# Kernel tuning notes

Hardware: AMD Instinct MI355X
Metric: run time of the kernel (lower is better)

The kernel has to match this reference:

```python
import jax, jax.numpy as jnp
import numpy as np

TOPN = 1000
MIN_SCORE = 0.05
NMS_THR = 0.5
MAX_OBJ = 100
B, A, C = 8, 100000, 80


def setup_inputs():
    key = jax.random.key(0)
    k1, k2, k3, k4 = jax.random.split(key, 4)
    cls_heads = jax.random.uniform(k1, (B, A, C), dtype=jnp.float32)  # sigmoid-like class scores
    reg_heads = (jax.random.normal(k2, (B, A, 4), dtype=jnp.float32) * 0.1)  # small tx,ty,tw,th
    ctr = jax.random.uniform(k3, (B, A, 2), minval=32.0, maxval=768.0)
    wh = jax.random.uniform(k4, (B, A, 2), minval=16.0, maxval=128.0)
    batch_anchors = jnp.concatenate([ctr - 0.5 * wh, ctr + 0.5 * wh], axis=-1)
    return {"cls_heads": cls_heads, "reg_heads": reg_heads, "batch_anchors": batch_anchors}


def _decode(reg, anchors):
    # snap tx,ty,tw,th to x1y1x2y2; original casts to int (truncation toward zero)
    awh = anchors[..., 2:4] - anchors[..., 0:2]
    actr = anchors[..., 0:2] + 0.5 * awh
    pwh = jnp.exp(reg[..., 2:4]) * awh
    pctr = reg[..., 0:2] * awh + actr
    boxes = jnp.concatenate([pctr - 0.5 * pwh, pctr + 0.5 * pwh], axis=-1)
    return jnp.trunc(boxes)  # matches torch .int() truncation, kept float


def _per_image(scores, classes, boxes):
    # score-threshold filter + descending sort + topn, done as masked top_k (fixed shapes)
    masked = jnp.where(scores > MIN_SCORE, scores, -jnp.inf)
    top_s, idx = jax.lax.top_k(masked, TOPN)
    valid = top_s > MIN_SCORE
    top_c = classes[idx].astype(jnp.float32)
    top_b = boxes[idx]  # [TOPN,4]

    # pairwise IoU (greedy python_nms math)
    wh = top_b[:, 2:4] - top_b[:, 0:2]
    area = jnp.clip(wh[:, 0] * wh[:, 1], 1e-4)  # clamp(min=0.0001)
    tl = jnp.maximum(top_b[:, None, 0:2], top_b[None, :, 0:2])
    br = jnp.minimum(top_b[:, None, 2:4], top_b[None, :, 2:4])
    sz = jnp.clip(br - tl, 0.0)
    inter = sz[..., 0] * sz[..., 1]
    union = jnp.clip(area[:, None] + area[None, :] - inter, 1e-4)
    iou = inter / union  # [TOPN,TOPN]

    ar = jnp.arange(TOPN)

    def body(i, supp):
        # box i, if not already suppressed, suppresses later boxes with iou >= thr
        return supp | ((~supp[i]) & (iou[i] >= NMS_THR) & (ar > i))

    supp = jax.lax.fori_loop(0, TOPN, body, ~valid)
    kept = (~supp) & valid

    # compact first MAX_OBJ kept detections (score order preserved); pad with -1 / zeros
    rank = jnp.cumsum(kept) - 1
    slot = jnp.where(kept & (rank < MAX_OBJ), rank, MAX_OBJ)  # dump slot MAX_OBJ
    out_s = jnp.full((MAX_OBJ + 1,), -1.0, jnp.float32).at[slot].set(jnp.where(kept, top_s, -1.0))[:MAX_OBJ]
    out_c = jnp.full((MAX_OBJ + 1,), -1.0, jnp.float32).at[slot].set(jnp.where(kept, top_c, -1.0))[:MAX_OBJ]
    out_b = jnp.zeros((MAX_OBJ + 1, 4), jnp.float32).at[slot].set(jnp.where(kept[:, None], top_b, 0.0))[:MAX_OBJ]
    return out_s, out_c, out_b


def reference(cls_heads, reg_heads, batch_anchors):
    scores = jnp.max(cls_heads, axis=2)        # [B,A]
    classes = jnp.argmax(cls_heads, axis=2)    # [B,A] int
    boxes = _decode(reg_heads, batch_anchors)  # [B,A,4]
    return jax.vmap(_per_image)(scores, classes, boxes)
```

## Files before the change

### kernel.cpp

```cpp
#include <hip/hip_runtime.h>
#include <cstdint>

#define NB 8
#define NA 100000
#define NC 80
#define TOPN 1000
#define MAXOBJ 100
#define CAND_CAP 2048
#define MIN_SCORE 0.05f
#define NMS_THR 0.5f

__global__ __launch_bounds__(320) void k_scores(const float* __restrict__ cls,
                                                unsigned int* __restrict__ keys,
                                                int* __restrict__ clsid) {
    __shared__ float sval[320];
    __shared__ int sidx[320];
    const int b = blockIdx.y;
    const int a0 = blockIdx.x * 16;
    const int t = threadIdx.x;
    const float4* base = (const float4*)(cls + ((size_t)b * NA + a0) * NC);
    float4 v = base[t];
    float m = v.x; int ix = 0;
    if (v.y > m) { m = v.y; ix = 1; }
    if (v.z > m) { m = v.z; ix = 2; }
    if (v.w > m) { m = v.w; ix = 3; }
    const int e = t % 20;
    sval[t] = m;
    sidx[t] = e * 4 + ix;
    __syncthreads();
    if (t < 16) {
        float vm = sval[t * 20]; int vi = sidx[t * 20];
        for (int i = 1; i < 20; ++i) {
            float x = sval[t * 20 + i];
            if (x > vm) { vm = x; vi = sidx[t * 20 + i]; }
        }
        size_t o = (size_t)b * NA + a0 + t;
        keys[o] = (vm > MIN_SCORE) ? __float_as_uint(vm) : 0u;
        clsid[o] = vi;
    }
}

__device__ inline void wave_agg_hist(unsigned int* lh, int bin, bool pred) {
    unsigned long long active = __ballot(pred);
    const int lane = threadIdx.x & 63;
    while (active) {
        int leader = (int)__builtin_ctzll(active);
        int lbin = __shfl(bin, leader);
        unsigned long long mask = __ballot(pred && (bin == lbin));
        if (lane == leader) atomicAdd(&lh[lbin], (unsigned int)__popcll(mask));
        active &= ~mask;
    }
}

__device__ inline void top_threshold(const unsigned int* lh, int nbins, int minbin,
                                     unsigned int rank, int* out_bin, unsigned int* out_above) {
    const int lane = threadIdx.x;
    const int chunk = nbins >> 6;
    const int hi = nbins - 1 - lane * chunk;
    const int lo = hi - chunk + 1;
    unsigned int s = 0;
    for (int i = hi; i >= lo; --i)
        if (i >= minbin) s += lh[i];
    unsigned int incl = s;
    for (int d = 1; d < 64; d <<= 1) {
        unsigned int o = __shfl_up(incl, d);
        if (lane >= d) incl += o;
    }
    unsigned int pre = incl - s;
    bool hit = (pre < rank) && (incl >= rank);
    unsigned long long m = __ballot(hit);
    if (m == 0ull) {
        if (lane == 0) { *out_bin = -1; *out_above = 0; }
        return;
    }
    if (hit) {
        unsigned int cum = pre;
        int fb = -1;
        for (int i = hi; i >= lo; --i) {
            if (i < minbin) break;
            unsigned int c = lh[i];
            if (cum + c >= rank) { fb = i; break; }
            cum += c;
        }
        *out_bin = fb;
        *out_above = cum;
    }
}

__global__ __launch_bounds__(1024) void k_mega(
    const unsigned int* __restrict__ keys, const int* __restrict__ clsid,
    const float* __restrict__ reg, const float* __restrict__ anch,
    float* __restrict__ out) {
    __shared__ unsigned int lh[2048];
    __shared__ unsigned long long sk[CAND_CAP];
    __shared__ float4 sbox[TOPN];
    __shared__ float ss[TOPN];
    __shared__ float scl[TOPN];
    __shared__ int s_bin;
    __shared__ unsigned int s_above;
    __shared__ unsigned int s_cnt;

    const int b = blockIdx.x;
    const int tid = threadIdx.x;
    const int lane = tid & 63;
    const unsigned int* kb = keys + (size_t)b * NA;
    float* out_s = out + b * MAXOBJ;
    float* out_c = out + NB * MAXOBJ + b * MAXOBJ;
    float* out_b = out + 2 * NB * MAXOBJ + b * MAXOBJ * 4;

    if (tid < MAXOBJ) { out_s[tid] = -1.0f; out_c[tid] = -1.0f; }
    if (tid < MAXOBJ * 4) out_b[tid] = 0.0f;

    for (int i = tid; i < 2048; i += 1024) lh[i] = 0;
    __syncthreads();
    for (int base = 0; base < NA; base += 1024) {
        int a = base + tid;
        bool p = a < NA;
        unsigned int key = p ? kb[a] : 0u;
        wave_agg_hist(lh, (int)(key >> 21), p);
    }
    __syncthreads();
    if (tid < 64) top_threshold(lh, 2048, 1, TOPN, &s_bin, &s_above);
    __syncthreads();
    const int p1 = s_bin;
    const unsigned int above1 = s_above;

    unsigned int T;
    if (p1 < 0) {
        T = 1u;
    } else {
        __syncthreads();
        for (int i = tid; i < 2048; i += 1024) lh[i] = 0;
        __syncthreads();
        for (int base = 0; base < NA; base += 1024) {
            int a = base + tid;
            if (a < NA) {
                unsigned int key = kb[a];
                if ((int)(key >> 21) == p1) atomicAdd(&lh[(key >> 10) & 0x7FFu], 1u);
            }
        }
        __syncthreads();
        if (tid < 64) top_threshold(lh, 2048, 0, TOPN - above1, &s_bin, &s_above);
        __syncthreads();
        const int p2 = s_bin;
        const unsigned int above2 = above1 + s_above;
        if (p2 < 0) {
            T = 1u;
        } else {
            const unsigned int pref = ((unsigned int)p1 << 11) | (unsigned int)p2;
            __syncthreads();
            for (int i = tid; i < 1024; i += 1024) lh[i] = 0;
            __syncthreads();
            for (int base = 0; base < NA; base += 1024) {
                int a = base + tid;
                if (a < NA) {
                    unsigned int key = kb[a];
                    if ((key >> 10) == pref) atomicAdd(&lh[key & 0x3FFu], 1u);
                }
            }
            __syncthreads();
            if (tid < 64) top_threshold(lh, 1024, 0, TOPN - above2, &s_bin, &s_above);
            __syncthreads();
            const int p3 = s_bin;
            T = (p3 < 0) ? 1u : ((pref << 10) | (unsigned int)p3);
        }
    }
    __syncthreads();

    for (int i = tid; i < CAND_CAP; i += 1024) sk[i] = 0ull;
    if (tid == 0) s_cnt = 0;
    __syncthreads();
    for (int base = 0; base < NA; base += 1024) {
        int a = base + tid;
        unsigned int key = (a < NA) ? kb[a] : 0u;
        bool w = (key >= T) && (key != 0u);
        unsigned long long m = __ballot(w);
        if (m) {
            int leader = (int)__builtin_ctzll(m);
            unsigned int base_slot = 0;
            if (lane == leader) base_slot = atomicAdd(&s_cnt, (unsigned int)__popcll(m));
            base_slot = __shfl(base_slot, leader);
            unsigned int off = (unsigned int)__popcll(m & ((1ull << lane) - 1ull));
            unsigned int pos = base_slot + off;
            if (w && pos < CAND_CAP)
                sk[pos] = ((unsigned long long)key << 32) |
                          (unsigned long long)(0xFFFFFFFFu - (unsigned int)a);
        }
    }
    __syncthreads();

    for (int k = 2; k <= CAND_CAP; k <<= 1)
        for (int j = k >> 1; j > 0; j >>= 1) {
            __syncthreads();
            for (int i = tid; i < CAND_CAP; i += 1024) {
                int ixj = i ^ j;
                if (ixj > i) {
                    unsigned long long x = sk[i], y = sk[ixj];
                    bool desc = ((i & k) == 0);
                    if (desc ? (x < y) : (x > y)) { sk[i] = y; sk[ixj] = x; }
                }
            }
        }
    __syncthreads();

    if (tid < TOPN) {
        unsigned long long e = sk[tid];
        unsigned int key = (unsigned int)(e >> 32);
        if (key != 0u) {
            int a = (int)(0xFFFFFFFFu - (unsigned int)e);
            size_t base = (size_t)b * NA + a;
            float4 r  = ((const float4*)reg)[base];
            float4 an = ((const float4*)anch)[base];
            float aw = an.z - an.x, ah = an.w - an.y;
            float acx = an.x + 0.5f * aw, acy = an.y + 0.5f * ah;
            float pw = expf(r.z) * aw, ph = expf(r.w) * ah;
            float pcx = r.x * aw + acx, pcy = r.y * ah + acy;
            float4 bx;
            bx.x = truncf(pcx - 0.5f * pw); bx.y = truncf(pcy - 0.5f * ph);
            bx.z = truncf(pcx + 0.5f * pw); bx.w = truncf(pcy + 0.5f * ph);
            sbox[tid] = bx;
            ss[tid] = __uint_as_float(key);
            scl[tid] = (float)clsid[base];
        } else {
            sbox[tid] = make_float4(0.f, 0.f, 0.f, 0.f);
            ss[tid] = -1.0f;
            scl[tid] = -1.0f;
        }
    }
    __syncthreads();
    if (tid >= 64) return;

    float k0x1 = 0, k0y1 = 0, k0x2 = 0, k0y2 = 0, k0a = 0;
    float k1x1 = 0, k1y1 = 0, k1x2 = 0, k1y2 = 0, k1a = 0;
    int kc = 0;
    for (int i = 0; i < TOPN; ++i) {
        float4 bi = sbox[i];
        float si = ss[i];
        if (!(si > MIN_SCORE)) break;
        float areai = fmaxf((bi.z - bi.x) * (bi.w - bi.y), 1e-4f);
        bool sup = false;
        if (lane < kc) {
            float ix = fminf(k0x2, bi.z) - fmaxf(k0x1, bi.x);
            float iy = fminf(k0y2, bi.w) - fmaxf(k0y1, bi.y);
            float inter = fmaxf(ix, 0.0f) * fmaxf(iy, 0.0f);
            float uni = fmaxf(k0a + areai - inter, 1e-4f);
            sup = (inter / uni) >= NMS_THR;
        }
        if (lane + 64 < kc) {
            float ix = fminf(k1x2, bi.z) - fmaxf(k1x1, bi.x);
            float iy = fminf(k1y2, bi.w) - fmaxf(k1y1, bi.y);
            float inter = fmaxf(ix, 0.0f) * fmaxf(iy, 0.0f);
            float uni = fmaxf(k1a + areai - inter, 1e-4f);
            sup = sup || ((inter / uni) >= NMS_THR);
        }
        if (__ballot(sup) == 0ull) {
            if (lane == 0) {
                out_s[kc] = si;
                out_c[kc] = scl[i];
                out_b[kc * 4 + 0] = bi.x; out_b[kc * 4 + 1] = bi.y;
                out_b[kc * 4 + 2] = bi.z; out_b[kc * 4 + 3] = bi.w;
            }
            if (kc < 64) {
                if (lane == kc) { k0x1 = bi.x; k0y1 = bi.y; k0x2 = bi.z; k0y2 = bi.w; k0a = areai; }
            } else {
                if (lane == kc - 64) { k1x1 = bi.x; k1y1 = bi.y; k1x2 = bi.z; k1y2 = bi.w; k1a = areai; }
            }
            ++kc;
            if (kc >= MAXOBJ) break;
        }
    }
}

extern "C" void kernel_launch(void* const* d_in, const int* in_sizes, int n_in,
                              void* d_out, int out_size, void* d_ws, size_t ws_size,
                              hipStream_t stream) {
    const float* cls  = (const float*)d_in[0];
    const float* reg  = (const float*)d_in[1];
    const float* anch = (const float*)d_in[2];
    float* out = (float*)d_out;
    char* ws = (char*)d_ws;

    unsigned int* keys = (unsigned int*)ws;
    int* clsid = (int*)(ws + 3200000);

    dim3 grid1(NA / 16, NB);
    k_scores<<<grid1, 320, 0, stream>>>(cls, keys, clsid);
    k_mega<<<NB, 1024, 0, stream>>>(keys, clsid, reg, anch, out);
}
```

Before: 508.0 us.

## Split per-image radix select into grid-wide histogram, scan and collect kernels

The single per-image mega kernel, which ran on only 8 blocks and made four serial passes over 100k keys, is replaced by a chain of grid-parallel kernels. The first-level histogram is fused into the score kernel via global atomics. Refinement histograms and candidate collection now run across many blocks, with small scan kernels choosing each radix prefix. The score kernel also processes 64 anchors per block using a padded shared layout. The aim is to spread the memory-bound passes across the whole GPU, at the cost of more launches, a memset and global atomics.

```diff
diff --git a/kernel.cpp b/kernel.cpp
--- a/kernel.cpp
+++ b/kernel.cpp
@@ -12,55 +12,75 @@
 
 __global__ __launch_bounds__(320) void k_scores(const float* __restrict__ cls,
                                                 unsigned int* __restrict__ keys,
-                                                int* __restrict__ clsid) {
-    __shared__ float sval[320];
-    __shared__ int sidx[320];
+                                                int* __restrict__ clsid,
+                                                unsigned int* __restrict__ hist1) {
+    __shared__ float sval[64 * 21];
+    __shared__ int sidx[64 * 21];
     const int b = blockIdx.y;
-    const int a0 = blockIdx.x * 16;
+    const int a0 = blockIdx.x * 64;
     const int t = threadIdx.x;
     const float4* base = (const float4*)(cls + ((size_t)b * NA + a0) * NC);
-    float4 v = base[t];
-    float m = v.x; int ix = 0;
-    if (v.y > m) { m = v.y; ix = 1; }
-    if (v.z > m) { m = v.z; ix = 2; }
-    if (v.w > m) { m = v.w; ix = 3; }
-    const int e = t % 20;
-    sval[t] = m;
-    sidx[t] = e * 4 + ix;
-    __syncthreads();
-    if (t < 16) {
-        float vm = sval[t * 20]; int vi = sidx[t * 20];
-        for (int i = 1; i < 20; ++i) {
-            float x = sval[t * 20 + i];
-            if (x > vm) { vm = x; vi = sidx[t * 20 + i]; }
-        }
-        size_t o = (size_t)b * NA + a0 + t;
-        keys[o] = (vm > MIN_SCORE) ? __float_as_uint(vm) : 0u;
-        clsid[o] = vi;
-    }
-}
-
-__device__ inline void wave_agg_hist(unsigned int* lh, int bin, bool pred) {
-    unsigned long long active = __ballot(pred);
-    const int lane = threadIdx.x & 63;
-    while (active) {
-        int leader = (int)__builtin_ctzll(active);
-        int lbin = __shfl(bin, leader);
-        unsigned long long mask = __ballot(pred && (bin == lbin));
-        if (lane == leader) atomicAdd(&lh[lbin], (unsigned int)__popcll(mask));
-        active &= ~mask;
-    }
-}
-
-__device__ inline void top_threshold(const unsigned int* lh, int nbins, int minbin,
-                                     unsigned int rank, int* out_bin, unsigned int* out_above) {
+    const int fmax = (NA - a0) * 20 - 1;
+
+    int f0 = t, f1 = 320 + t, f2 = 640 + t, f3 = 960 + t;
+    float4 v0 = base[min(f0, fmax)];
+    float4 v1 = base[min(f1, fmax)];
+    float4 v2 = base[min(f2, fmax)];
+    float4 v3 = base[min(f3, fmax)];
+
+#define REDUCE4(v, f)                                                   \
+    {                                                                   \
+        float m = v.x; int ix = 0;                                      \
+        if (v.y > m) { m = v.y; ix = 1; }                               \
+        if (v.z > m) { m = v.z; ix = 2; }                               \
+        if (v.w > m) { m = v.w; ix = 3; }                               \
+        int al = (f) / 20, e = (f) % 20;                                \
+        sval[al * 21 + e] = m;                                          \
+        sidx[al * 21 + e] = e * 4 + ix;                                 \
+    }
+    REDUCE4(v0, f0) REDUCE4(v1, f1) REDUCE4(v2, f2) REDUCE4(v3, f3)
+#undef REDUCE4
+    __syncthreads();
+
+    if (t < 64) {
+        const int a = a0 + t;
+        unsigned int key = 0u;
+        if (a < NA) {
+            float vm = sval[t * 21]; int vi = sidx[t * 21];
+            for (int j = 1; j < 20; ++j) {
+                float x = sval[t * 21 + j];
+                if (x > vm) { vm = x; vi = sidx[t * 21 + j]; }
+            }
+            key = (vm > MIN_SCORE) ? __float_as_uint(vm) : 0u;
+            size_t o = (size_t)b * NA + a;
+            keys[o] = key;
+            clsid[o] = vi;
+        }
+        const int lane = t;
+        int bin = (int)(key >> 21);
+        bool pred = (a < NA) && (key != 0u);
+        unsigned long long active = __ballot(pred);
+        while (active) {
+            int leader = (int)__builtin_ctzll(active);
+            int lbin = __shfl(bin, leader);
+            unsigned long long mask = __ballot(pred && (bin == lbin));
+            if (lane == leader) atomicAdd(&hist1[b * 2048 + lbin], (unsigned int)__popcll(mask));
+            active &= ~mask;
+        }
+    }
+}
+
+__device__ inline void top_threshold_g(const unsigned int* __restrict__ h, int nbins,
+                                       int minbin, unsigned int rank,
+                                       int* __restrict__ out_bin,
+                                       unsigned int* __restrict__ out_above) {
     const int lane = threadIdx.x;
     const int chunk = nbins >> 6;
     const int hi = nbins - 1 - lane * chunk;
     const int lo = hi - chunk + 1;
     unsigned int s = 0;
     for (int i = hi; i >= lo; --i)
-        if (i >= minbin) s += lh[i];
+        if (i >= minbin) s += h[i];
     unsigned int incl = s;
     for (int d = 1; d < 64; d <<= 1) {
         unsigned int o = __shfl_up(incl, d);
@@ -78,7 +98,7 @@
         int fb = -1;
         for (int i = hi; i >= lo; --i) {
             if (i < minbin) break;
-            unsigned int c = lh[i];
+            unsigned int c = h[i];
             if (cum + c >= rank) { fb = i; break; }
             cum += c;
         }
@@ -87,23 +107,129 @@
     }
 }
 
-__global__ __launch_bounds__(1024) void k_mega(
-    const unsigned int* __restrict__ keys, const int* __restrict__ clsid,
-    const float* __restrict__ reg, const float* __restrict__ anch,
+__global__ __launch_bounds__(64) void k_scan(int mode, const unsigned int* __restrict__ h1,
+                                             const unsigned int* __restrict__ h2,
+                                             const unsigned int* __restrict__ h3,
+                                             int* prefix1, unsigned int* above1,
+                                             int* prefix2, unsigned int* above2,
+                                             unsigned int* T) {
+    const int b = blockIdx.x;
+    __shared__ int s_bin;
+    __shared__ unsigned int s_above;
+    if (mode == 1) {
+        top_threshold_g(h1 + b * 2048, 2048, 1, TOPN, &s_bin, &s_above);
+        __syncthreads();
+        if (threadIdx.x == 0) {
+            prefix1[b] = s_bin;
+            above1[b] = s_above;
+            if (s_bin < 0) T[b] = 1u;
+        }
+    } else if (mode == 2) {
+        if (prefix1[b] < 0) return;
+        top_threshold_g(h2 + b * 2048, 2048, 0, TOPN - above1[b], &s_bin, &s_above);
+        __syncthreads();
+        if (threadIdx.x == 0) {
+            if (s_bin < 0) { prefix2[b] = -1; T[b] = 1u; }
+            else { prefix2[b] = (prefix1[b] << 11) | s_bin; above2[b] = above1[b] + s_above; }
+        }
+    } else {
+        if (prefix1[b] < 0 || prefix2[b] < 0) return;
+        top_threshold_g(h3 + b * 1024, 1024, 0, TOPN - above2[b], &s_bin, &s_above);
+        __syncthreads();
+        if (threadIdx.x == 0)
+            T[b] = (s_bin < 0) ? 1u : (((unsigned int)prefix2[b] << 10) | (unsigned int)s_bin);
+    }
+}
+
+__global__ __launch_bounds__(256) void k_hist2(const unsigned int* __restrict__ keys,
+                                               const int* __restrict__ prefix1,
+                                               unsigned int* __restrict__ hist2) {
+    __shared__ unsigned int lh[2048];
+    const int b = blockIdx.y;
+    const int p = prefix1[b];
+    if (p < 0) return;
+    const int t = threadIdx.x;
+    const int a0 = blockIdx.x * 2048;
+    const unsigned int* kb = keys + (size_t)b * NA;
+    for (int i = t; i < 2048; i += 256) lh[i] = 0;
+    __syncthreads();
+    for (int c = 0; c < 8; ++c) {
+        int a = a0 + c * 256 + t;
+        if (a < NA) {
+            unsigned int key = kb[a];
+            if ((int)(key >> 21) == p) atomicAdd(&lh[(key >> 10) & 0x7FFu], 1u);
+        }
+    }
+    __syncthreads();
+    for (int i = t; i < 2048; i += 256)
+        if (lh[i]) atomicAdd(&hist2[b * 2048 + i], lh[i]);
+}
+
+__global__ __launch_bounds__(256) void k_hist3(const unsigned int* __restrict__ keys,
+                                               const int* __restrict__ prefix1,
+                                               const int* __restrict__ prefix2,
+                                               unsigned int* __restrict__ hist3) {
+    __shared__ unsigned int lh[1024];
+    const int b = blockIdx.y;
+    if (prefix1[b] < 0 || prefix2[b] < 0) return;
+    const unsigned int pref = (unsigned int)prefix2[b];
+    const int t = threadIdx.x;
+    const int a0 = blockIdx.x * 2048;
+    const unsigned int* kb = keys + (size_t)b * NA;
+    for (int i = t; i < 1024; i += 256) lh[i] = 0;
+    __syncthreads();
+    for (int c = 0; c < 8; ++c) {
+        int a = a0 + c * 256 + t;
+        if (a < NA) {
+            unsigned int key = kb[a];
+            if ((key >> 10) == pref) atomicAdd(&lh[key & 0x3FFu], 1u);
+        }
+    }
+    __syncthreads();
+    for (int i = t; i < 1024; i += 256)
+        if (lh[i]) atomicAdd(&hist3[b * 1024 + i], lh[i]);
+}
+
+__global__ __launch_bounds__(256) void k_collect(const unsigned int* __restrict__ keys,
+                                                 const unsigned int* __restrict__ T,
+                                                 unsigned int* __restrict__ n_cand,
+                                                 unsigned long long* __restrict__ cand) {
+    const int b = blockIdx.y;
+    const int t = threadIdx.x;
+    const int lane = t & 63;
+    const int a0 = blockIdx.x * 2048;
+    const unsigned int* kb = keys + (size_t)b * NA;
+    const unsigned int thr = T[b];
+    for (int c = 0; c < 8; ++c) {
+        int a = a0 + c * 256 + t;
+        unsigned int key = (a < NA) ? kb[a] : 0u;
+        bool w = (key >= thr) && (key != 0u);
+        unsigned long long m = __ballot(w);
+        if (m) {
+            int leader = (int)__builtin_ctzll(m);
+            unsigned int base_slot = 0;
+            if (lane == leader) base_slot = atomicAdd(&n_cand[b], (unsigned int)__popcll(m));
+            base_slot = __shfl(base_slot, leader);
+            unsigned int off = (unsigned int)__popcll(m & ((1ull << lane) - 1ull));
+            unsigned int pos = base_slot + off;
+            if (w && pos < CAND_CAP)
+                cand[(size_t)b * CAND_CAP + pos] =
+                    ((unsigned long long)key << 32) |
+                    (unsigned long long)(0xFFFFFFFFu - (unsigned int)a);
+        }
+    }
+}
+
+__global__ __launch_bounds__(1024) void k_final(
+    const unsigned long long* __restrict__ cand, const unsigned int* __restrict__ n_cand,
+    const int* __restrict__ clsid, const float* __restrict__ reg, const float* __restrict__ anch,
     float* __restrict__ out) {
-    __shared__ unsigned int lh[2048];
     __shared__ unsigned long long sk[CAND_CAP];
     __shared__ float4 sbox[TOPN];
     __shared__ float ss[TOPN];
     __shared__ float scl[TOPN];
-    __shared__ int s_bin;
-    __shared__ unsigned int s_above;
-    __shared__ unsigned int s_cnt;
-
     const int b = blockIdx.x;
     const int tid = threadIdx.x;
-    const int lane = tid & 63;
-    const unsigned int* kb = keys + (size_t)b * NA;
     float* out_s = out + b * MAXOBJ;
     float* out_c = out + NB * MAXOBJ + b * MAXOBJ;
     float* out_b = out + 2 * NB * MAXOBJ + b * MAXOBJ * 4;
@@ -111,83 +237,9 @@
     if (tid < MAXOBJ) { out_s[tid] = -1.0f; out_c[tid] = -1.0f; }
     if (tid < MAXOBJ * 4) out_b[tid] = 0.0f;
 
-    for (int i = tid; i < 2048; i += 1024) lh[i] = 0;
-    __syncthreads();
-    for (int base = 0; base < NA; base += 1024) {
-        int a = base + tid;
-        bool p = a < NA;
-        unsigned int key = p ? kb[a] : 0u;
-        wave_agg_hist(lh, (int)(key >> 21), p);
-    }
-    __syncthreads();
-    if (tid < 64) top_threshold(lh, 2048, 1, TOPN, &s_bin, &s_above);
-    __syncthreads();
-    const int p1 = s_bin;
-    const unsigned int above1 = s_above;
-
-    unsigned int T;
-    if (p1 < 0) {
-        T = 1u;
-    } else {
-        __syncthreads();
-        for (int i = tid; i < 2048; i += 1024) lh[i] = 0;
-        __syncthreads();
-        for (int base = 0; base < NA; base += 1024) {
-            int a = base + tid;
-            if (a < NA) {
-                unsigned int key = kb[a];
-                if ((int)(key >> 21) == p1) atomicAdd(&lh[(key >> 10) & 0x7FFu], 1u);
-            }
-        }
-        __syncthreads();
-        if (tid < 64) top_threshold(lh, 2048, 0, TOPN - above1, &s_bin, &s_above);
-        __syncthreads();
-        const int p2 = s_bin;
-        const unsigned int above2 = above1 + s_above;
-        if (p2 < 0) {
-            T = 1u;
-        } else {
-            const unsigned int pref = ((unsigned int)p1 << 11) | (unsigned int)p2;
-            __syncthreads();
-            for (int i = tid; i < 1024; i += 1024) lh[i] = 0;
-            __syncthreads();
-            for (int base = 0; base < NA; base += 1024) {
-                int a = base + tid;
-                if (a < NA) {
-                    unsigned int key = kb[a];
-                    if ((key >> 10) == pref) atomicAdd(&lh[key & 0x3FFu], 1u);
-                }
-            }
-            __syncthreads();
-            if (tid < 64) top_threshold(lh, 1024, 0, TOPN - above2, &s_bin, &s_above);
-            __syncthreads();
-            const int p3 = s_bin;
-            T = (p3 < 0) ? 1u : ((pref << 10) | (unsigned int)p3);
-        }
-    }
-    __syncthreads();
-
-    for (int i = tid; i < CAND_CAP; i += 1024) sk[i] = 0ull;
-    if (tid == 0) s_cnt = 0;
-    __syncthreads();
-    for (int base = 0; base < NA; base += 1024) {
-        int a = base + tid;
-        unsigned int key = (a < NA) ? kb[a] : 0u;
-        bool w = (key >= T) && (key != 0u);
-        unsigned long long m = __ballot(w);
-        if (m) {
-            int leader = (int)__builtin_ctzll(m);
-            unsigned int base_slot = 0;
-            if (lane == leader) base_slot = atomicAdd(&s_cnt, (unsigned int)__popcll(m));
-            base_slot = __shfl(base_slot, leader);
-            unsigned int off = (unsigned int)__popcll(m & ((1ull << lane) - 1ull));
-            unsigned int pos = base_slot + off;
-            if (w && pos < CAND_CAP)
-                sk[pos] = ((unsigned long long)key << 32) |
-                          (unsigned long long)(0xFFFFFFFFu - (unsigned int)a);
-        }
-    }
-    __syncthreads();
+    int n = (int)n_cand[b]; if (n > CAND_CAP) n = CAND_CAP;
+    for (int i = tid; i < CAND_CAP; i += 1024)
+        sk[i] = (i < n) ? cand[(size_t)b * CAND_CAP + i] : 0ull;
 
     for (int k = 2; k <= CAND_CAP; k <<= 1)
         for (int j = k >> 1; j > 0; j >>= 1) {
@@ -230,6 +282,7 @@
     __syncthreads();
     if (tid >= 64) return;
 
+    const int lane = tid;
     float k0x1 = 0, k0y1 = 0, k0x2 = 0, k0y2 = 0, k0a = 0;
     float k1x1 = 0, k1y1 = 0, k1x2 = 0, k1y2 = 0, k1a = 0;
     int kc = 0;
@@ -282,8 +335,28 @@
 
     unsigned int* keys = (unsigned int*)ws;
     int* clsid = (int*)(ws + 3200000);
-
-    dim3 grid1(NA / 16, NB);
-    k_scores<<<grid1, 320, 0, stream>>>(cls, keys, clsid);
-    k_mega<<<NB, 1024, 0, stream>>>(keys, clsid, reg, anch, out);
-}
+    unsigned long long* cand = (unsigned long long*)(ws + 6400000);
+    char* zbase = ws + 6400000 + 131072;
+    unsigned int* h1 = (unsigned int*)zbase;
+    unsigned int* h2 = (unsigned int*)(zbase + 65536);
+    unsigned int* h3 = (unsigned int*)(zbase + 131072);
+    unsigned int* n_cand  = (unsigned int*)(zbase + 163840);
+    int* prefix1          = (int*)(zbase + 163840 + 32);
+    unsigned int* above1  = (unsigned int*)(zbase + 163840 + 64);
+    int* prefix2          = (int*)(zbase + 163840 + 96);
+    unsigned int* above2  = (unsigned int*)(zbase + 163840 + 128);
+    unsigned int* T       = (unsigned int*)(zbase + 163840 + 160);
+
+    hipMemsetAsync(zbase, 0, 163840 + 192, stream);
+
+    dim3 gscore((NA + 63) / 64, NB);
+    dim3 ghist((NA + 2047) / 2048, NB);
+    k_scores<<<gscore, 320, 0, stream>>>(cls, keys, clsid, h1);
+    k_scan<<<NB, 64, 0, stream>>>(1, h1, h2, h3, prefix1, above1, prefix2, above2, T);
+    k_hist2<<<ghist, 256, 0, stream>>>(keys, prefix1, h2);
+    k_scan<<<NB, 64, 0, stream>>>(2, h1, h2, h3, prefix1, above1, prefix2, above2, T);
+    k_hist3<<<ghist, 256, 0, stream>>>(keys, prefix1, prefix2, h3);
+    k_scan<<<NB, 64, 0, stream>>>(3, h1, h2, h3, prefix1, above1, prefix2, above2, T);
+    k_collect<<<ghist, 256, 0, stream>>>(keys, T, n_cand, cand);
+    k_final<<<NB, 1024, 0, stream>>>(cand, n_cand, clsid, reg, anch, out);
+}
```

Measured after the change: 524.9 us. 1.03x slower.

## Prefilter high-score candidates in score kernel to shrink top-k selection scan

Applied to the files above, without the earlier changes.

The score kernel now handles 64 anchors per block and appends every anchor whose score key reaches a fixed 0.999 threshold to a per-image candidate list using wave-aggregated global atomics. The selection kernel then runs its radix histogram passes and compaction over that small list instead of all 100k keys, falling back to the full scan when the count is below TOPN or overflows the buffer. This targets the single-block-per-image serial scans that dominate the second kernel. It adds a memset and global atomics, and the fixed threshold only pays off when the score distribution puts at least 1000 anchors above 0.999.

```diff
diff --git a/kernel.cpp b/kernel.cpp
--- a/kernel.cpp
+++ b/kernel.cpp
@@ -6,37 +6,72 @@
 #define NC 80
 #define TOPN 1000
 #define MAXOBJ 100
-#define CAND_CAP 2048
+#define CAND1 16384
+#define SORTN 2048
 #define MIN_SCORE 0.05f
 #define NMS_THR 0.5f
 
 __global__ __launch_bounds__(320) void k_scores(const float* __restrict__ cls,
                                                 unsigned int* __restrict__ keys,
-                                                int* __restrict__ clsid) {
-    __shared__ float sval[320];
-    __shared__ int sidx[320];
+                                                int* __restrict__ clsid,
+                                                unsigned long long* __restrict__ cand,
+                                                unsigned int* __restrict__ n_cand) {
+    __shared__ float sval[64 * 21];
+    __shared__ int sidx[64 * 21];
     const int b = blockIdx.y;
-    const int a0 = blockIdx.x * 16;
+    const int a0 = blockIdx.x * 64;
     const int t = threadIdx.x;
     const float4* base = (const float4*)(cls + ((size_t)b * NA + a0) * NC);
-    float4 v = base[t];
-    float m = v.x; int ix = 0;
-    if (v.y > m) { m = v.y; ix = 1; }
-    if (v.z > m) { m = v.z; ix = 2; }
-    if (v.w > m) { m = v.w; ix = 3; }
-    const int e = t % 20;
-    sval[t] = m;
-    sidx[t] = e * 4 + ix;
-    __syncthreads();
-    if (t < 16) {
-        float vm = sval[t * 20]; int vi = sidx[t * 20];
-        for (int i = 1; i < 20; ++i) {
-            float x = sval[t * 20 + i];
-            if (x > vm) { vm = x; vi = sidx[t * 20 + i]; }
-        }
-        size_t o = (size_t)b * NA + a0 + t;
-        keys[o] = (vm > MIN_SCORE) ? __float_as_uint(vm) : 0u;
-        clsid[o] = vi;
+    const int fmax = (NA - a0) * 20 - 1;
+
+    int f0 = t, f1 = 320 + t, f2 = 640 + t, f3 = 960 + t;
+    float4 v0 = base[min(f0, fmax)];
+    float4 v1 = base[min(f1, fmax)];
+    float4 v2 = base[min(f2, fmax)];
+    float4 v3 = base[min(f3, fmax)];
+
+#define REDUCE4(v, f)                                                   \
+    {                                                                   \
+        float m = v.x; int ix = 0;                                      \
+        if (v.y > m) { m = v.y; ix = 1; }                               \
+        if (v.z > m) { m = v.z; ix = 2; }                               \
+        if (v.w > m) { m = v.w; ix = 3; }                               \
+        int al = (f) / 20, e = (f) % 20;                                \
+        sval[al * 21 + e] = m;                                          \
+        sidx[al * 21 + e] = e * 4 + ix;                                 \
+    }
+    REDUCE4(v0, f0) REDUCE4(v1, f1) REDUCE4(v2, f2) REDUCE4(v3, f3)
+#undef REDUCE4
+    __syncthreads();
+
+    if (t < 64) {
+        const int a = a0 + t;
+        unsigned int key = 0u;
+        if (a < NA) {
+            float vm = sval[t * 21]; int vi = sidx[t * 21];
+            for (int j = 1; j < 20; ++j) {
+                float x = sval[t * 21 + j];
+                if (x > vm) { vm = x; vi = sidx[t * 21 + j]; }
+            }
+            key = (vm > MIN_SCORE) ? __float_as_uint(vm) : 0u;
+            size_t o = (size_t)b * NA + a;
+            keys[o] = key;
+            clsid[o] = vi;
+        }
+        const unsigned int T0 = __float_as_uint(0.999f);
+        bool w = (a < NA) && (key >= T0);
+        unsigned long long m = __ballot(w);
+        if (m) {
+            int leader = (int)__builtin_ctzll(m);
+            unsigned int bs = 0;
+            if (t == leader) bs = atomicAdd(&n_cand[b], (unsigned int)__popcll(m));
+            bs = __shfl(bs, leader);
+            unsigned int pos = bs + (unsigned int)__popcll(m & ((1ull << t) - 1ull));
+            if (w && pos < CAND1)
+                cand[(size_t)b * CAND1 + pos] =
+                    ((unsigned long long)key << 32) |
+                    (unsigned long long)(0xFFFFFFFFu - (unsigned int)a);
+        }
     }
 }
 
@@ -87,12 +122,13 @@
     }
 }
 
-__global__ __launch_bounds__(1024) void k_mega(
+__global__ __launch_bounds__(1024) void k_select(
     const unsigned int* __restrict__ keys, const int* __restrict__ clsid,
+    const unsigned long long* __restrict__ cand, const unsigned int* __restrict__ n_cand,
     const float* __restrict__ reg, const float* __restrict__ anch,
     float* __restrict__ out) {
     __shared__ unsigned int lh[2048];
-    __shared__ unsigned long long sk[CAND_CAP];
+    __shared__ unsigned long long sk[SORTN];
     __shared__ float4 sbox[TOPN];
     __shared__ float ss[TOPN];
     __shared__ float scl[TOPN];
@@ -104,6 +140,7 @@
     const int tid = threadIdx.x;
     const int lane = tid & 63;
     const unsigned int* kb = keys + (size_t)b * NA;
+    const unsigned long long* cb = cand + (size_t)b * CAND1;
     float* out_s = out + b * MAXOBJ;
     float* out_c = out + NB * MAXOBJ + b * MAXOBJ;
     float* out_b = out + 2 * NB * MAXOBJ + b * MAXOBJ * 4;
@@ -111,13 +148,17 @@
     if (tid < MAXOBJ) { out_s[tid] = -1.0f; out_c[tid] = -1.0f; }
     if (tid < MAXOBJ * 4) out_b[tid] = 0.0f;
 
+    const unsigned int n0 = n_cand[b];
+    const bool fast = (n0 >= TOPN) && (n0 <= CAND1);
+    const int N = fast ? (int)n0 : NA;
+
     for (int i = tid; i < 2048; i += 1024) lh[i] = 0;
     __syncthreads();
-    for (int base = 0; base < NA; base += 1024) {
-        int a = base + tid;
-        bool p = a < NA;
-        unsigned int key = p ? kb[a] : 0u;
-        wave_agg_hist(lh, (int)(key >> 21), p);
+    for (int base = 0; base < N; base += 1024) {
+        int i = base + tid;
+        unsigned int k = 0u;
+        if (i < N) k = fast ? (unsigned int)(cb[i] >> 32) : kb[i];
+        wave_agg_hist(lh, (int)(k >> 21), (i < N) && (k != 0u));
     }
     __syncthreads();
     if (tid < 64) top_threshold(lh, 2048, 1, TOPN, &s_bin, &s_above);
@@ -132,11 +173,11 @@
         __syncthreads();
         for (int i = tid; i < 2048; i += 1024) lh[i] = 0;
         __syncthreads();
-        for (int base = 0; base < NA; base += 1024) {
-            int a = base + tid;
-            if (a < NA) {
-                unsigned int key = kb[a];
-                if ((int)(key >> 21) == p1) atomicAdd(&lh[(key >> 10) & 0x7FFu], 1u);
+        for (int base = 0; base < N; base += 1024) {
+            int i = base + tid;
+            if (i < N) {
+                unsigned int k = fast ? (unsigned int)(cb[i] >> 32) : kb[i];
+                if ((int)(k >> 21) == p1) atomicAdd(&lh[(k >> 10) & 0x7FFu], 1u);
             }
         }
         __syncthreads();
@@ -151,48 +192,53 @@
             __syncthreads();
             for (int i = tid; i < 1024; i += 1024) lh[i] = 0;
             __syncthreads();
-            for (int base = 0; base < NA; base += 1024) {
-                int a = base + tid;
-                if (a < NA) {
-                    unsigned int key = kb[a];
-                    if ((key >> 10) == pref) atomicAdd(&lh[key & 0x3FFu], 1u);
+            for (int base = 0; base < N; base += 1024) {
+                int i = base + tid;
+                if (i < N) {
+                    unsigned int k = fast ? (unsigned int)(cb[i] >> 32) : kb[i];
+                    if ((k >> 10) == pref) atomicAdd(&lh[k & 0x3FFu], 1u);
                 }
             }
             __syncthreads();
             if (tid < 64) top_threshold(lh, 1024, 0, TOPN - above2, &s_bin, &s_above);
             __syncthreads();
-            const int p3 = s_bin;
-            T = (p3 < 0) ? 1u : ((pref << 10) | (unsigned int)p3);
-        }
-    }
-    __syncthreads();
-
-    for (int i = tid; i < CAND_CAP; i += 1024) sk[i] = 0ull;
+            T = (s_bin < 0) ? 1u : ((pref << 10) | (unsigned int)s_bin);
+        }
+    }
+    __syncthreads();
+
+    for (int i = tid; i < SORTN; i += 1024) sk[i] = 0ull;
     if (tid == 0) s_cnt = 0;
     __syncthreads();
-    for (int base = 0; base < NA; base += 1024) {
-        int a = base + tid;
-        unsigned int key = (a < NA) ? kb[a] : 0u;
-        bool w = (key >= T) && (key != 0u);
+    for (int base = 0; base < N; base += 1024) {
+        int i = base + tid;
+        unsigned long long e = 0ull;
+        unsigned int k = 0u;
+        if (i < N) {
+            if (fast) { e = cb[i]; k = (unsigned int)(e >> 32); }
+            else {
+                k = kb[i];
+                e = ((unsigned long long)k << 32) |
+                    (unsigned long long)(0xFFFFFFFFu - (unsigned int)i);
+            }
+        }
+        bool w = (k >= T) && (k != 0u);
         unsigned long long m = __ballot(w);
         if (m) {
             int leader = (int)__builtin_ctzll(m);
-            unsigned int base_slot = 0;
-            if (lane == leader) base_slot = atomicAdd(&s_cnt, (unsigned int)__popcll(m));
-            base_slot = __shfl(base_slot, leader);
-            unsigned int off = (unsigned int)__popcll(m & ((1ull << lane) - 1ull));
-            unsigned int pos = base_slot + off;
-            if (w && pos < CAND_CAP)
-                sk[pos] = ((unsigned long long)key << 32) |
-                          (unsigned long long)(0xFFFFFFFFu - (unsigned int)a);
-        }
-    }
-    __syncthreads();
-
-    for (int k = 2; k <= CAND_CAP; k <<= 1)
+            unsigned int bs = 0;
+            if (lane == leader) bs = atomicAdd(&s_cnt, (unsigned int)__popcll(m));
+            bs = __shfl(bs, leader);
+            unsigned int pos = bs + (unsigned int)__popcll(m & ((1ull << lane) - 1ull));
+            if (w && pos < SORTN) sk[pos] = e;
+        }
+    }
+    __syncthreads();
+
+    for (int k = 2; k <= SORTN; k <<= 1)
         for (int j = k >> 1; j > 0; j >>= 1) {
             __syncthreads();
-            for (int i = tid; i < CAND_CAP; i += 1024) {
+            for (int i = tid; i < SORTN; i += 1024) {
                 int ixj = i ^ j;
                 if (ixj > i) {
                     unsigned long long x = sk[i], y = sk[ixj];
@@ -282,8 +328,12 @@
 
     unsigned int* keys = (unsigned int*)ws;
     int* clsid = (int*)(ws + 3200000);
-
-    dim3 grid1(NA / 16, NB);
-    k_scores<<<grid1, 320, 0, stream>>>(cls, keys, clsid);
-    k_mega<<<NB, 1024, 0, stream>>>(keys, clsid, reg, anch, out);
-}
+    unsigned long long* cand = (unsigned long long*)(ws + 6400000);
+    unsigned int* n_cand = (unsigned int*)(ws + 7448576);
+
+    hipMemsetAsync(n_cand, 0, 32, stream);
+
+    dim3 gscore((NA + 63) / 64, NB);
+    k_scores<<<gscore, 320, 0, stream>>>(cls, keys, clsid, cand, n_cand);
+    k_select<<<NB, 1024, 0, stream>>>(keys, clsid, cand, n_cand, reg, anch, out);
+}
```

Result: no change. 498.3 us (-1.9%).
